# Optimization experiments

Measured on AMD Instinct MI355X. Metric: run time of the kernel, lower is better.

The kernel has to match this reference:

```python
import jax, jax.numpy as jnp
import numpy as np

U, I, F, E = 100_000, 50_000, 64, 1_600_000


def setup_inputs() -> dict:
    key = jax.random.key(0)
    k1, k2, k3, k4, k5, k6 = jax.random.split(key, 6)
    users_embedding = jax.random.normal(k1, (U, F), dtype=jnp.float32) * 0.01
    items_embedding = jax.random.normal(k2, (I, F), dtype=jnp.float32) * 0.01
    # COO edge list of the bipartite user-item graph; values play the role of
    # the (normalized) nonzeros of user_item_matrix / item_user_matrix.
    edge_user = jax.random.randint(k3, (E,), 0, U, dtype=jnp.int32)
    edge_item = jax.random.randint(k4, (E,), 0, I, dtype=jnp.int32)
    ui_vals = jax.random.uniform(k5, (E,), dtype=jnp.float32) * 0.1
    iu_vals = jax.random.uniform(k6, (E,), dtype=jnp.float32) * 0.1
    return {
        "users_embedding": users_embedding,
        "items_embedding": items_embedding,
        "ui_vals": ui_vals,
        "iu_vals": iu_vals,
        "edge_user": edge_user,
        "edge_item": edge_item,
    }


def reference(users_embedding, items_embedding, ui_vals, iu_vals, edge_user, edge_item):
    n_users = users_embedding.shape[0]
    n_items = items_embedding.shape[0]

    def spmm_ui(x):  # user_item_matrix @ x, x: [I, F] -> [U, F]
        return jax.ops.segment_sum(ui_vals[:, None] * x[edge_item], edge_user,
                                   num_segments=n_users)

    def spmm_iu(x):  # item_user_matrix @ x, x: [U, F] -> [I, F]
        return jax.ops.segment_sum(iu_vals[:, None] * x[edge_user], edge_item,
                                   num_segments=n_items)

    gcn1_u = spmm_ui(items_embedding) + users_embedding
    gcn1_i = spmm_iu(users_embedding) + items_embedding
    gcn2_u = spmm_ui(gcn1_i) + gcn1_u
    gcn2_i = spmm_iu(gcn1_u) + gcn1_i
    # NOTE: the original code computes gcn3_* but does NOT include them in the
    # concatenated output, so we skip that dead computation.
    gcn_users = jnp.concatenate([users_embedding, gcn1_u, gcn2_u], axis=-1)  # [U, 3F]
    gcn_items = jnp.concatenate([items_embedding, gcn1_i, gcn2_i], axis=-1)  # [I, 3F]
    return (gcn_users, gcn_items)
```

## Files before the change

### kernel.cpp

```cpp
#include <hip/hip_runtime.h>


typedef unsigned long long ull;

#define TILE   8192
#define MAX_NB 2048
#define CAP    3072

__device__ inline ushort f2bf(float x) {
    unsigned u = __float_as_uint(x);
    return (ushort)((u + 0x7FFF + ((u >> 16) & 1)) >> 16);
}
__device__ inline int pack15(float x) {
    unsigned u = __float_as_uint(x);
    return (int)(((u + 0x7FFF + ((u >> 16) & 1)) >> 16) & 0x7FFF);
}
__device__ inline unsigned char f2e4m3(float x) {
    unsigned u = __float_as_uint(x);
    unsigned s = (u >> 24) & 0x80u;
    u &= 0x7FFFFFFFu;
    if (u < 0x3C000000u) return (unsigned char)s;
    u += 0x7FFFFu + ((u >> 20) & 1u);
    int e = (int)(u >> 23) - 120;
    unsigned m = (u >> 20) & 7u;
    unsigned q;
    if (e >= 16 || (e == 15 && m == 7)) q = 0x7Eu;
    else if (e <= 0) q = 0u;
    else q = ((unsigned)e << 3) | m;
    return (unsigned char)(q | s);
}
__device__ inline float e4m3_to_f32(unsigned b) {
#if __has_builtin(__builtin_amdgcn_cvt_f32_fp8)
    return __builtin_amdgcn_cvt_f32_fp8((int)b, 0);
#else
    if (!(b & 0x7Fu)) return 0.f;
    unsigned f = ((b & 0x80u) << 24) | (((b & 0x7Fu) << 20) + (120u << 23));
    return __uint_as_float(f);
#endif
}

__global__ __launch_bounds__(1024) void bin_kernel(
    const int* __restrict__ eu, const int* __restrict__ ei,
    const float* __restrict__ uiv, const float* __restrict__ iuv,
    int* __restrict__ gwp, int2* __restrict__ scv,
    int E, int nb_u, int nb)
{
    __shared__ int cnt[MAX_NB];
    __shared__ int base[MAX_NB];
    int t0 = blockIdx.x * TILE;
    int n  = min(TILE, E - t0);
    for (int b = threadIdx.x; b < nb; b += 1024) cnt[b] = 0;
    __syncthreads();
    for (int k = threadIdx.x; k < n; k += 1024) {
        atomicAdd(&cnt[eu[t0 + k] >> 7], 1);
        atomicAdd(&cnt[nb_u + (ei[t0 + k] >> 6)], 1);
    }
    __syncthreads();
    for (int b = threadIdx.x; b < nb; b += 1024) {
        int c = cnt[b];
        base[b] = c ? (b * CAP + atomicAdd(&gwp[b], c)) : 0;
        cnt[b] = 0;
    }
    __syncthreads();
    for (int k = threadIdx.x; k < n; k += 1024) {
        int u = eu[t0 + k], it = ei[t0 + k];
        int bu = u >> 7;
        int pu = base[bu] + atomicAdd(&cnt[bu], 1);
        scv[pu] = make_int2(((u & 127) << 24) | it, pack15(uiv[t0 + k]));
        int bi = nb_u + (it >> 6);
        int pi = base[bi] + atomicAdd(&cnt[bi], 1);
        scv[pi] = make_int2(((it & 63) << 24) | u, pack15(iuv[t0 + k]));
    }
}

__global__ __launch_bounds__(256) void place_kernel(
    const int* __restrict__ gwp, const int2* __restrict__ scv,
    unsigned* __restrict__ cv, int2* __restrict__ rpe_u, int2* __restrict__ rpe_i,
    int nb_u, int U, int I)
{
    __shared__ int2 cvL[CAP];
    __shared__ int cnt[128];
    __shared__ int wp[128];
    int b = blockIdx.x;
    bool uside = (b < nb_u);
    int rl2   = uside ? 7 : 6;
    int row0  = (uside ? b : b - nb_u) << rl2;
    int ntot  = uside ? U : I;
    int nr    = min(1 << rl2, ntot - row0);
    int2* rpo = uside ? rpe_u : rpe_i;
    int bbase = b * CAP;
    int n = min(gwp[b], CAP);
    int t = threadIdx.x;

    if (t < 128) cnt[t] = 0;
    for (int k = t; k < n; k += 256) cvL[k] = scv[bbase + k];
    __syncthreads();
    for (int k = t; k < n; k += 256)
        atomicAdd(&cnt[(unsigned)cvL[k].x >> 24], 1);
    __syncthreads();

    int x = (t < 128) ? cnt[t] : 0;
    if (t < 128) wp[t] = x;
    __syncthreads();
    #pragma unroll
    for (int o = 1; o < 128; o <<= 1) {
        int v = (t < 128 && t >= o) ? wp[t - o] : 0;
        __syncthreads();
        if (t < 128) wp[t] += v;
        __syncthreads();
    }
    int incl = (t < 128) ? wp[t] : 0;
    int excl = incl - x;
    if (t < 128) wp[t] = excl;
    if (t < nr) rpo[row0 + t] = make_int2(bbase + excl, bbase + incl);
    __syncthreads();

    for (int k = t; k < n; k += 256) {
        int2 w = cvL[k];
        int r = (unsigned)w.x >> 24;
        int dst = bbase + atomicAdd(&wp[r], 1);
        cv[dst] = ((unsigned)w.y << 17) | ((unsigned)w.x & 0x1FFFF);
    }
}

__global__ void conv2_kernel(const float4* __restrict__ a, ushort4* __restrict__ da16,
                             uchar4* __restrict__ da8, int n4a,
                             const float4* __restrict__ b, ushort4* __restrict__ db16,
                             uchar4* __restrict__ db8, int n4b)
{
    int i = blockIdx.x * blockDim.x + threadIdx.x;
    const float4* s; ushort4* d16; uchar4* d8; int j;
    if (i < n4a) { s = a; d16 = da16; d8 = da8; j = i; }
    else { j = i - n4a; if (j >= n4b) return; s = b; d16 = db16; d8 = db8; }
    float4 v = s[j];
    ushort4 o16;
    o16.x = f2bf(v.x); o16.y = f2bf(v.y); o16.z = f2bf(v.z); o16.w = f2bf(v.w);
    uchar4 o8;
    o8.x = f2e4m3(v.x * 512.f); o8.y = f2e4m3(v.y * 512.f);
    o8.z = f2e4m3(v.z * 512.f); o8.w = f2e4m3(v.w * 512.f);
    d16[j] = o16; d8[j] = o8;
}

template <int STAGE>
__global__ __launch_bounds__(256) void gather_stage(
    const int2* __restrict__ rpe_u, const int2* __restrict__ rpe_i,
    const unsigned* __restrict__ cv,
    const unsigned char* __restrict__ e8_u, const unsigned char* __restrict__ e8_i,
    const ushort* __restrict__ e16_u, const ushort* __restrict__ e16_i,
    unsigned char* __restrict__ g8_u, unsigned char* __restrict__ g8_i,
    ushort* __restrict__ g16_u, ushort* __restrict__ g16_i,
    float* __restrict__ out_u, float* __restrict__ out_i,
    int U, int I)
{
    int wid = (blockIdx.x * blockDim.x + threadIdx.x) >> 6;
    int f   = threadIdx.x & 63;
    if (wid >= U + I) return;

    const int2* rpe; float* outp;
    const unsigned char* src8; const ushort* res16;
    unsigned char* g8p; ushort* g16p; int row;
    if (wid < U) {
        row = wid; rpe = rpe_u; outp = out_u; g8p = g8_u; g16p = g16_u;
        src8  = (STAGE == 1) ? e8_i  : g8_i;
        res16 = (STAGE == 1) ? e16_u : g16_u;
    } else {
        row = wid - U; rpe = rpe_i; outp = out_i; g8p = g8_i; g16p = g16_i;
        src8  = (STAGE == 1) ? e8_u  : g8_u;
        res16 = (STAGE == 1) ? e16_i : g16_i;
    }

    int2 be = rpe[row];
    int beg = be.x, end = be.y;
    int n = end - beg;
    unsigned myc = (f < n) ? cv[beg + f] : 0u;
    float    myval  = __uint_as_float((myc >> 17) << 16) * (1.0f / 512.0f);
    unsigned myoffB = (myc & 0x1FFFF) << 6;
    const char* sbase = (const char*)src8 + (unsigned)f;
    int nn = min(n, 64);

    auto ld2 = [&](float v, unsigned oB) -> float {
        unsigned q = *(const unsigned char*)(sbase + oB);
        return v * e4m3_to_f32(q);
    };

    float a0 = 0.f, a1 = 0.f, a2 = 0.f, a3 = 0.f;
    float a4 = 0.f, a5 = 0.f, a6 = 0.f, a7 = 0.f;
    int e = 0;
    for (; e + 7 < nn; e += 8) {
        float    v0 = __shfl(myval, e),      v1 = __shfl(myval, e + 1);
        float    v2 = __shfl(myval, e + 2),  v3 = __shfl(myval, e + 3);
        float    v4 = __shfl(myval, e + 4),  v5 = __shfl(myval, e + 5);
        float    v6 = __shfl(myval, e + 6),  v7 = __shfl(myval, e + 7);
        unsigned o0 = __shfl(myoffB, e),     o1 = __shfl(myoffB, e + 1);
        unsigned o2 = __shfl(myoffB, e + 2), o3 = __shfl(myoffB, e + 3);
        unsigned o4 = __shfl(myoffB, e + 4), o5 = __shfl(myoffB, e + 5);
        unsigned o6 = __shfl(myoffB, e + 6), o7 = __shfl(myoffB, e + 7);
        a0 += ld2(v0, o0); a1 += ld2(v1, o1); a2 += ld2(v2, o2); a3 += ld2(v3, o3);
        a4 += ld2(v4, o4); a5 += ld2(v5, o5); a6 += ld2(v6, o6); a7 += ld2(v7, o7);
    }
    for (; e < nn; ++e)
        a0 += ld2(__shfl(myval, e), __shfl(myoffB, e));
    for (int k = beg + 64; k < end; ++k) {
        unsigned c = cv[k];
        a0 += ld2(__uint_as_float((c >> 17) << 16) * (1.0f / 512.0f),
                  (c & 0x1FFFF) << 6);
    }

    float acc = ((a0 + a1) + (a2 + a3)) + ((a4 + a5) + (a6 + a7));
    float res = __uint_as_float((unsigned)res16[row * 64 + f] << 16);
    acc += res;
    if (STAGE == 1) {
        __builtin_nontemporal_store(res, &outp[row * 192 + f]);
        __builtin_nontemporal_store(acc, &outp[row * 192 + 64 + f]);
        g16p[row * 64 + f] = f2bf(acc);
        g8p[row * 64 + f]  = f2e4m3(acc * 512.f);
    } else {
        __builtin_nontemporal_store(acc, &outp[row * 192 + 128 + f]);
    }
}

__global__ void init_dup_kernel(const float4* __restrict__ src,
                                float4* __restrict__ dst, int nrows)
{
    int gid = blockIdx.x * blockDim.x + threadIdx.x;
    if (gid >= nrows * 16) return;
    int row = gid >> 4, c = gid & 15;
    float4 v = src[gid];
    dst[row * 48 + c]      = v;
    dst[row * 48 + 16 + c] = v;
}
__global__ void copy_col_kernel(float4* __restrict__ buf, int nrows)
{
    int gid = blockIdx.x * blockDim.x + threadIdx.x;
    if (gid >= nrows * 16) return;
    int row = gid >> 4, c = gid & 15;
    buf[row * 48 + 32 + c] = buf[row * 48 + 16 + c];
}
__global__ void spmm_atomic(const int* __restrict__ eu, const int* __restrict__ ei,
                            const float* __restrict__ uiv, const float* __restrict__ iuv,
                            const float* __restrict__ su, int ssu,
                            const float* __restrict__ si, int ssi,
                            float* __restrict__ ou, float* __restrict__ oi,
                            int dst_col, int E)
{
    int gid = blockIdx.x * blockDim.x + threadIdx.x;
    if (gid >= E * 64) return;
    int e = gid >> 6, f = gid & 63;
    int u = eu[e], i = ei[e];
    unsafeAtomicAdd(&ou[u * 192 + dst_col + f], uiv[e] * si[i * ssi + f]);
    unsafeAtomicAdd(&oi[i * 192 + dst_col + f], iuv[e] * su[u * ssu + f]);
}

extern "C" void kernel_launch(void* const* d_in, const int* in_sizes, int n_in,
                              void* d_out, int out_size, void* d_ws, size_t ws_size,
                              hipStream_t stream)
{
    const float* emb_u   = (const float*)d_in[0];
    const float* emb_i   = (const float*)d_in[1];
    const float* ui_vals = (const float*)d_in[2];
    const float* iu_vals = (const float*)d_in[3];
    const int*   e_user  = (const int*)d_in[4];
    const int*   e_item  = (const int*)d_in[5];

    const int F = 64;
    const int U = in_sizes[0] / F;
    const int I = in_sizes[1] / F;
    const int E = in_sizes[4];

    float* out_u = (float*)d_out;
    float* out_i = out_u + (size_t)U * 192;

    const int BLK = 256;
    int nb_u = (U + 127) >> 7;
    int nb_i = (I + 63) >> 6;
    int nb   = nb_u + nb_i;

    char* base = (char*)d_ws;
    size_t off = 0;
    auto alloc = [&](size_t bytes, size_t align) -> char* {
        off = (off + align - 1) & ~(align - 1);
        char* p = base + off;
        off += bytes;
        return p;
    };
    int*  gwp   = (int*)alloc((size_t)nb * 4, 4);
    int2* rpe_u = (int2*)alloc((size_t)U * 8, 8);
    int2* rpe_i = (int2*)alloc((size_t)I * 8, 8);
    unsigned* cv = (unsigned*)alloc((size_t)nb * CAP * 4, 8);
    int2* scv   = (int2*)alloc((size_t)nb * CAP * 8, 8);
    ushort* g16_u = (ushort*)alloc((size_t)U * 64 * 2, 8);
    ushort* g16_i = (ushort*)alloc((size_t)I * 64 * 2, 8);
    size_t need = off;

    char* ovl = (char*)scv;
    ushort* e16_u = (ushort*)ovl;
    ushort* e16_i = e16_u + (size_t)U * 64;
    unsigned char* e8_u = (unsigned char*)(ovl + (size_t)(U + I) * 128);
    unsigned char* e8_i = e8_u + (size_t)U * 64;
    unsigned char* g8_u = e8_i + (size_t)I * 64;
    unsigned char* g8_i = g8_u + (size_t)U * 64;
    bool ovl_fits = ((size_t)(U + I) * 256) <= (size_t)nb * CAP * 8;
    bool cols_fit = (U < (1 << 17)) && (I < (1 << 17));
    bool cap_ok = ((size_t)2 * E / (size_t)nb) <= (CAP * 2 / 3);

    if (ws_size < need || nb > MAX_NB || !ovl_fits || !cols_fit || !cap_ok) {
        int grid_u = (U * 16 + BLK - 1) / BLK;
        int grid_i = (I * 16 + BLK - 1) / BLK;
        long long tt = (long long)E * 64;
        int grid_e = (int)((tt + BLK - 1) / BLK);
        init_dup_kernel<<<grid_u, BLK, 0, stream>>>((const float4*)emb_u, (float4*)out_u, U);
        init_dup_kernel<<<grid_i, BLK, 0, stream>>>((const float4*)emb_i, (float4*)out_i, I);
        spmm_atomic<<<grid_e, BLK, 0, stream>>>(e_user, e_item, ui_vals, iu_vals,
                                                emb_u, 64, emb_i, 64, out_u, out_i, 64, E);
        copy_col_kernel<<<grid_u, BLK, 0, stream>>>((float4*)out_u, U);
        copy_col_kernel<<<grid_i, BLK, 0, stream>>>((float4*)out_i, I);
        spmm_atomic<<<grid_e, BLK, 0, stream>>>(e_user, e_item, ui_vals, iu_vals,
                                                out_u + 64, 192, out_i + 64, 192,
                                                out_u, out_i, 128, E);
        return;
    }

    int ntiles = (E + TILE - 1) / TILE;

    hipMemsetAsync(gwp, 0, (size_t)nb * 4, stream);
    bin_kernel<<<ntiles, 1024, 0, stream>>>(e_user, e_item, ui_vals, iu_vals,
                                            gwp, scv, E, nb_u, nb);
    place_kernel<<<nb, BLK, 0, stream>>>(gwp, scv, cv, rpe_u, rpe_i, nb_u, U, I);

    int n4u = U * 16, n4i = I * 16;
    conv2_kernel<<<(n4u + n4i + BLK - 1) / BLK, BLK, 0, stream>>>(
        (const float4*)emb_u, (ushort4*)e16_u, (uchar4*)e8_u, n4u,
        (const float4*)emb_i, (ushort4*)e16_i, (uchar4*)e8_i, n4i);

    int grid_g = ((U + I) * 64 + BLK - 1) / BLK;
    gather_stage<1><<<grid_g, BLK, 0, stream>>>(
        rpe_u, rpe_i, cv, e8_u, e8_i, e16_u, e16_i,
        g8_u, g8_i, g16_u, g16_i, out_u, out_i, U, I);
    gather_stage<2><<<grid_g, BLK, 0, stream>>>(
        rpe_u, rpe_i, cv, e8_u, e8_i, e16_u, e16_i,
        g8_u, g8_i, g16_u, g16_i, out_u, out_i, U, I);
}
```

Before: 255.5 us.

## Split SpMM wavefront into 4 edge groups with dword fp8 gathers

Each 64-lane wavefront now handles 4 edges at a time instead of one: 16 lanes per edge, each lane loading 4 packed fp8 features as a single dword and unpacking them with packed fp8-to-f32 conversion. The four partial sums are combined with xor shuffles across lane groups, and the epilogue stores are vectorized and spread across the groups. This cuts the number of byte-sized gather instructions and shuffles per edge, at the cost of a cross-lane reduction and less unrolled independent accumulation. The scalar fp8 fallback builtin is also removed.

```diff
diff --git a/kernel.cpp b/kernel.cpp
--- a/kernel.cpp
+++ b/kernel.cpp
@@ -2,6 +2,8 @@
 
 
 typedef unsigned long long ull;
+typedef float __attribute__((ext_vector_type(2))) floatx2;
+typedef float __attribute__((ext_vector_type(4))) floatx4;
 
 #define TILE   8192
 #define MAX_NB 2048
@@ -10,6 +12,9 @@
 __device__ inline ushort f2bf(float x) {
     unsigned u = __float_as_uint(x);
     return (ushort)((u + 0x7FFF + ((u >> 16) & 1)) >> 16);
+}
+__device__ inline float bf2f(ushort b) {
+    return __uint_as_float((unsigned)b << 16);
 }
 __device__ inline int pack15(float x) {
     unsigned u = __float_as_uint(x);
@@ -30,13 +35,9 @@
     return (unsigned char)(q | s);
 }
 __device__ inline float e4m3_to_f32(unsigned b) {
-#if __has_builtin(__builtin_amdgcn_cvt_f32_fp8)
-    return __builtin_amdgcn_cvt_f32_fp8((int)b, 0);
-#else
     if (!(b & 0x7Fu)) return 0.f;
     unsigned f = ((b & 0x80u) << 24) | (((b & 0x7Fu) << 20) + (120u << 23));
     return __uint_as_float(f);
-#endif
 }
 
 __global__ __launch_bounds__(1024) void bin_kernel(
@@ -175,47 +176,78 @@
     unsigned myc = (f < n) ? cv[beg + f] : 0u;
     float    myval  = __uint_as_float((myc >> 17) << 16) * (1.0f / 512.0f);
     unsigned myoffB = (myc & 0x1FFFF) << 6;
-    const char* sbase = (const char*)src8 + (unsigned)f;
+    int g  = f >> 4;
+    int fl = f & 15;
+    const char* sbase = (const char*)src8 + ((unsigned)fl << 2);
     int nn = min(n, 64);
 
-    auto ld2 = [&](float v, unsigned oB) -> float {
-        unsigned q = *(const unsigned char*)(sbase + oB);
-        return v * e4m3_to_f32(q);
+    floatx4 acc = {0.f, 0.f, 0.f, 0.f};
+    auto step = [&](int e) {
+        int idx = e + g;
+        float    v  = __shfl(myval, idx);
+        unsigned oB = __shfl(myoffB, idx);
+        unsigned q  = *(const unsigned*)(sbase + oB);
+#if __has_builtin(__builtin_amdgcn_cvt_pk_f32_fp8)
+        floatx2 lo = __builtin_amdgcn_cvt_pk_f32_fp8((int)q, false);
+        floatx2 hi = __builtin_amdgcn_cvt_pk_f32_fp8((int)q, true);
+        acc.x += v * lo[0]; acc.y += v * lo[1];
+        acc.z += v * hi[0]; acc.w += v * hi[1];
+#else
+        acc.x += v * e4m3_to_f32(q & 0xFF);
+        acc.y += v * e4m3_to_f32((q >> 8) & 0xFF);
+        acc.z += v * e4m3_to_f32((q >> 16) & 0xFF);
+        acc.w += v * e4m3_to_f32(q >> 24);
+#endif
     };
-
-    float a0 = 0.f, a1 = 0.f, a2 = 0.f, a3 = 0.f;
-    float a4 = 0.f, a5 = 0.f, a6 = 0.f, a7 = 0.f;
     int e = 0;
-    for (; e + 7 < nn; e += 8) {
-        float    v0 = __shfl(myval, e),      v1 = __shfl(myval, e + 1);
-        float    v2 = __shfl(myval, e + 2),  v3 = __shfl(myval, e + 3);
-        float    v4 = __shfl(myval, e + 4),  v5 = __shfl(myval, e + 5);
-        float    v6 = __shfl(myval, e + 6),  v7 = __shfl(myval, e + 7);
-        unsigned o0 = __shfl(myoffB, e),     o1 = __shfl(myoffB, e + 1);
-        unsigned o2 = __shfl(myoffB, e + 2), o3 = __shfl(myoffB, e + 3);
-        unsigned o4 = __shfl(myoffB, e + 4), o5 = __shfl(myoffB, e + 5);
-        unsigned o6 = __shfl(myoffB, e + 6), o7 = __shfl(myoffB, e + 7);
-        a0 += ld2(v0, o0); a1 += ld2(v1, o1); a2 += ld2(v2, o2); a3 += ld2(v3, o3);
-        a4 += ld2(v4, o4); a5 += ld2(v5, o5); a6 += ld2(v6, o6); a7 += ld2(v7, o7);
-    }
-    for (; e < nn; ++e)
-        a0 += ld2(__shfl(myval, e), __shfl(myoffB, e));
-    for (int k = beg + 64; k < end; ++k) {
+    for (; e + 15 < nn; e += 16) { step(e); step(e + 4); step(e + 8); step(e + 12); }
+    for (; e < nn; e += 4) step(e);
+    for (int k = beg + 64 + g; k < end; k += 4) {
         unsigned c = cv[k];
-        a0 += ld2(__uint_as_float((c >> 17) << 16) * (1.0f / 512.0f),
-                  (c & 0x1FFFF) << 6);
-    }
-
-    float acc = ((a0 + a1) + (a2 + a3)) + ((a4 + a5) + (a6 + a7));
-    float res = __uint_as_float((unsigned)res16[row * 64 + f] << 16);
-    acc += res;
+        float    v  = __uint_as_float((c >> 17) << 16) * (1.0f / 512.0f);
+        unsigned oB = (c & 0x1FFFF) << 6;
+        unsigned q  = *(const unsigned*)(sbase + oB);
+#if __has_builtin(__builtin_amdgcn_cvt_pk_f32_fp8)
+        floatx2 lo = __builtin_amdgcn_cvt_pk_f32_fp8((int)q, false);
+        floatx2 hi = __builtin_amdgcn_cvt_pk_f32_fp8((int)q, true);
+        acc.x += v * lo[0]; acc.y += v * lo[1];
+        acc.z += v * hi[0]; acc.w += v * hi[1];
+#else
+        acc.x += v * e4m3_to_f32(q & 0xFF);
+        acc.y += v * e4m3_to_f32((q >> 8) & 0xFF);
+        acc.z += v * e4m3_to_f32((q >> 16) & 0xFF);
+        acc.w += v * e4m3_to_f32(q >> 24);
+#endif
+    }
+
+    acc.x += __shfl_xor(acc.x, 16); acc.y += __shfl_xor(acc.y, 16);
+    acc.z += __shfl_xor(acc.z, 16); acc.w += __shfl_xor(acc.w, 16);
+    acc.x += __shfl_xor(acc.x, 32); acc.y += __shfl_xor(acc.y, 32);
+    acc.z += __shfl_xor(acc.z, 32); acc.w += __shfl_xor(acc.w, 32);
+
+    ushort4 r4 = *(const ushort4*)&res16[row * 64 + (fl << 2)];
+    floatx4 res = {bf2f(r4.x), bf2f(r4.y), bf2f(r4.z), bf2f(r4.w)};
+    floatx4 accr = {acc.x + res.x, acc.y + res.y, acc.z + res.z, acc.w + res.w};
+
     if (STAGE == 1) {
-        __builtin_nontemporal_store(res, &outp[row * 192 + f]);
-        __builtin_nontemporal_store(acc, &outp[row * 192 + 64 + f]);
-        g16p[row * 64 + f] = f2bf(acc);
-        g8p[row * 64 + f]  = f2e4m3(acc * 512.f);
+        if (g == 0) {
+            __builtin_nontemporal_store(accr, (floatx4*)&outp[row * 192 + 64 + (fl << 2)]);
+        } else if (g == 1) {
+            __builtin_nontemporal_store(res, (floatx4*)&outp[row * 192 + (fl << 2)]);
+        } else if (g == 2) {
+            ushort4 o;
+            o.x = f2bf(accr.x); o.y = f2bf(accr.y);
+            o.z = f2bf(accr.z); o.w = f2bf(accr.w);
+            *(ushort4*)&g16p[row * 64 + (fl << 2)] = o;
+        } else {
+            uchar4 o;
+            o.x = f2e4m3(accr.x * 512.f); o.y = f2e4m3(accr.y * 512.f);
+            o.z = f2e4m3(accr.z * 512.f); o.w = f2e4m3(accr.w * 512.f);
+            *(uchar4*)&g8p[row * 64 + (fl << 2)] = o;
+        }
     } else {
-        __builtin_nontemporal_store(acc, &outp[row * 192 + 128 + f]);
+        if (g == 0)
+            __builtin_nontemporal_store(accr, (floatx4*)&outp[row * 192 + 128 + (fl << 2)]);
     }
 }
 
```

New measurement: 220.8 us, median of 2. 13.6% less time.
